# Performance work log

Hardware: AMD Instinct MI355X
Metric: run time of the kernel (lower is better)

Reference implementation:

```python
import jax, jax.numpy as jnp
import numpy as np

N = 50000      # nodes
E = 400000     # edges
IN = 128       # in_channels
HID = 64       # hidden_channels (per head)
H = 4          # heads
OUT = 10       # classes
G = 64         # graphs in batch


def setup_inputs() -> dict:
    key = jax.random.key(0)
    ks = jax.random.split(key, 32)
    s = 0.05
    inp = {
        "x": jax.random.normal(ks[0], (N, IN), dtype=jnp.float32),
        "edge_index": jax.random.randint(ks[1], (2, E), 0, N, dtype=jnp.int32),
        "batch": jnp.sort(jax.random.randint(ks[2], (N,), 0, G, dtype=jnp.int32)),
    }
    # TransformerConv layer 1 params (in=IN -> heads*HID)
    d1 = H * HID
    inp["Wq1"] = jax.random.normal(ks[3], (IN, d1)) * s
    inp["bq1"] = jnp.zeros((d1,), jnp.float32)
    inp["Wk1"] = jax.random.normal(ks[4], (IN, d1)) * s
    inp["bk1"] = jnp.zeros((d1,), jnp.float32)
    inp["Wv1"] = jax.random.normal(ks[5], (IN, d1)) * s
    inp["bv1"] = jnp.zeros((d1,), jnp.float32)
    inp["Ws1"] = jax.random.normal(ks[6], (IN, d1)) * s   # root/skip weight
    inp["bs1"] = jnp.zeros((d1,), jnp.float32)
    # TransformerConv layer 2 params (in=H*HID -> heads*HID)
    inp["Wq2"] = jax.random.normal(ks[7], (d1, d1)) * s
    inp["bq2"] = jnp.zeros((d1,), jnp.float32)
    inp["Wk2"] = jax.random.normal(ks[8], (d1, d1)) * s
    inp["bk2"] = jnp.zeros((d1,), jnp.float32)
    inp["Wv2"] = jax.random.normal(ks[9], (d1, d1)) * s
    inp["bv2"] = jnp.zeros((d1,), jnp.float32)
    inp["Ws2"] = jax.random.normal(ks[10], (d1, d1)) * s
    inp["bs2"] = jnp.zeros((d1,), jnp.float32)
    # final classifier
    inp["Wl"] = jax.random.normal(ks[11], (d1, OUT)) * s
    inp["bl"] = jnp.zeros((OUT,), jnp.float32)
    return inp


def transformer_conv(x, src, dst, Wq, bq, Wk, bk, Wv, bv, Ws, bs):
    """PyG TransformerConv (concat=True, root_weight=True, beta=None, eval mode).
    src = edge_index[0] (source j), dst = edge_index[1] (target i).
    """
    n = x.shape[0]
    q = (x @ Wq + bq).reshape(n, H, HID)
    k = (x @ Wk + bk).reshape(n, H, HID)
    v = (x @ Wv + bv).reshape(n, H, HID)
    # per-edge attention logits [E, H]
    alpha = jnp.einsum('ehc,ehc->eh', q[dst], k[src]) / np.sqrt(HID).astype(np.float32)
    # scatter-softmax over incoming edges of each target node
    amax = jax.ops.segment_max(alpha, dst, num_segments=n)           # [N, H], -inf for isolated
    ex = jnp.exp(alpha - amax[dst])                                   # [E, H]
    denom = jax.ops.segment_sum(ex, dst, num_segments=n) + 1e-16      # [N, H]
    w = ex / denom[dst]                                               # normalized alpha [E, H]
    # scatter-sum aggregation of weighted values
    out = jax.ops.segment_sum(w[:, :, None] * v[src], dst, num_segments=n)  # [N, H, HID]
    out = out.reshape(n, H * HID)
    return out + (x @ Ws + bs)  # root/skip connection


def reference(x, edge_index, batch,
              Wq1, bq1, Wk1, bk1, Wv1, bv1, Ws1, bs1,
              Wq2, bq2, Wk2, bk2, Wv2, bv2, Ws2, bs2,
              Wl, bl):
    src, dst = edge_index[0], edge_index[1]
    h = jax.nn.elu(transformer_conv(x, src, dst, Wq1, bq1, Wk1, bk1, Wv1, bv1, Ws1, bs1))
    h = jax.nn.elu(transformer_conv(h, src, dst, Wq2, bq2, Wk2, bk2, Wv2, bv2, Ws2, bs2))
    # global mean pool per graph
    sums = jax.ops.segment_sum(h, batch, num_segments=G)              # [G, H*HID]
    cnt = jax.ops.segment_sum(jnp.ones((h.shape[0],), h.dtype), batch, num_segments=G)
    pooled = sums / jnp.maximum(cnt, 1.0)[:, None]
    logits = pooled @ Wl + bl
    return jax.nn.log_softmax(logits, axis=-1)
```

## Files before the change

kernel.cpp:

```cpp
#include <hip/hip_runtime.h>
#include <math.h>

constexpr int NN   = 50000;
constexpr int NE   = 400000;
constexpr int INC  = 128;
constexpr int NH   = 4;
constexpr int D1   = 256;
constexpr int D4   = 1024;
constexpr int NOUT = 10;
constexpr int NG   = 64;
constexpr int NB_SCAN = (NN + 255) / 256;


typedef __attribute__((ext_vector_type(8))) short bf16x8;
typedef __attribute__((ext_vector_type(4))) float f32x4;
typedef __attribute__((ext_vector_type(2))) float f32x2;

__device__ __forceinline__ short f2b(float f) {
  union { float f; unsigned int i; } v; v.f = f;
  unsigned int x = v.i;
  return (short)((x + 0x7FFFu + ((x >> 16) & 1u)) >> 16);
}
__device__ __forceinline__ float b2f(short u) {
  union { unsigned int i; float f; } v; v.i = ((unsigned int)(unsigned short)u) << 16;
  return v.f;
}
__device__ __forceinline__ float4 ld4b(const short* p) {
  short4 u = *(const short4*)p;
  return make_float4(b2f(u.x), b2f(u.y), b2f(u.z), b2f(u.w));
}
__device__ __forceinline__ int cvt_pk_bf16(float lo, float hi) {
  int r;
  asm volatile("v_cvt_pk_bf16_f32 %0, %1, %2" : "=v"(r) : "v"(lo), "v"(hi));
  return r;
}
__device__ __forceinline__ int pk_fp8x4(float a, float b, float c, float d) {
  int v = __builtin_amdgcn_cvt_pk_fp8_f32(a, b, 0, false);
  v = __builtin_amdgcn_cvt_pk_fp8_f32(c, d, v, true);
  return v;
}

__device__ __forceinline__ void gld_lds16(const short* g, short* l) {
  __builtin_amdgcn_global_load_lds(
      (const __attribute__((address_space(1))) unsigned int*)g,
      (__attribute__((address_space(3))) unsigned int*)l, 16, 0, 0);
}

constexpr int CVT_XB  = (NN * INC / 4 + 255) / 256;
constexpr int CVT_W1B = (4 * D1 * INC / 8 + 255) / 256;
constexpr int CVT_W2B = (4 * D1 * D1 / 8 + 255) / 256;
constexpr int CVT_BB  = 8;
constexpr int CVT_DB  = (NN + 255) / 256;
constexpr int CVT_FB  = 1;
constexpr int CVT_SB  = (NG * D1 + 255) / 256;

__device__ __forceinline__ void wt_one8(const float* Wq, const float* Wk,
    const float* Wv, const float* Ws, short* Wt, int kbits, int i) {
  const int K = 1 << kbits;
  const int row = i >> (kbits - 3);
  const int k0 = (i & ((K >> 3) - 1)) << 3;
  int seg, n;
  if (row < 256)      { seg = 0; n = row; }
  else if (row < 768) { int j = row - 256, off = j & 7;
                        seg = (off >= 4) ? 2 : 1; n = (j >> 3) * 4 + (off & 3); }
  else                { seg = 3; n = row - 768; }
  const float* W = (seg == 0) ? Wq : (seg == 1) ? Wk : (seg == 2) ? Wv : Ws;
  short o[8];
#pragma unroll
  for (int kk = 0; kk < 8; kk++) o[kk] = f2b(W[(size_t)(k0 + kk) * D1 + n]);
  int4 pk;
  short* ps = (short*)&pk;
#pragma unroll
  for (int kk = 0; kk < 8; kk++) ps[kk] = o[kk];
  *(int4*)(Wt + (size_t)row * K + k0) = pk;
}

__global__ void cvt_all_k(const float* __restrict__ x, short* __restrict__ Xb,
    const float* __restrict__ Wq1, const float* __restrict__ Wk1,
    const float* __restrict__ Wv1, const float* __restrict__ Ws1,
    const float* __restrict__ Wq2, const float* __restrict__ Wk2,
    const float* __restrict__ Wv2, const float* __restrict__ Ws2,
    short* __restrict__ Wtc1, short* __restrict__ Wtc2,
    const float* __restrict__ bq1, const float* __restrict__ bk1,
    const float* __restrict__ bv1, const float* __restrict__ bs1,
    const float* __restrict__ bq2, const float* __restrict__ bk2,
    const float* __restrict__ bv2, const float* __restrict__ bs2,
    float* __restrict__ bc1, float* __restrict__ bc2,
    int* __restrict__ deg, unsigned int* __restrict__ desc,
    float* __restrict__ sums) {
  const int b = blockIdx.x;
  const int t = threadIdx.x;
  if (b < CVT_XB) {
    int i = (b * 256 + t) * 4;
    if (i >= NN * INC) return;
    float4 v = *(const float4*)(x + i);
    short4 o; o.x = f2b(v.x); o.y = f2b(v.y); o.z = f2b(v.z); o.w = f2b(v.w);
    *(short4*)(Xb + i) = o;
  } else if (b < CVT_XB + CVT_W1B) {
    int i = (b - CVT_XB) * 256 + t;
    if (i < 4 * D1 * INC / 8) wt_one8(Wq1, Wk1, Wv1, Ws1, Wtc1, 7, i);
  } else if (b < CVT_XB + CVT_W1B + CVT_W2B) {
    int i = (b - CVT_XB - CVT_W1B) * 256 + t;
    if (i < 4 * D1 * D1 / 8) wt_one8(Wq2, Wk2, Wv2, Ws2, Wtc2, 8, i);
  } else if (b < CVT_XB + CVT_W1B + CVT_W2B + CVT_BB) {
    int i = (b - CVT_XB - CVT_W1B - CVT_W2B) * 256 + t;
    if (i >= 2 * D4) return;
    int row = i & (D4 - 1);
    const float* bq = (i < D4) ? bq1 : bq2;
    const float* bk = (i < D4) ? bk1 : bk2;
    const float* bv = (i < D4) ? bv1 : bv2;
    const float* bs = (i < D4) ? bs1 : bs2;
    float v;
    if (row < 256) v = bq[row];
    else if (row < 768) {
      int j = row - 256, grp = j >> 3, off = j & 7;
      int ch = grp * 4 + (off & 3);
      v = (off < 4) ? bk[ch] : bv[ch];
    } else v = bs[row - 768];
    ((i < D4) ? bc1 : bc2)[row] = v;
  } else if (b < CVT_XB + CVT_W1B + CVT_W2B + CVT_BB + CVT_DB) {
    int i = (b - CVT_XB - CVT_W1B - CVT_W2B - CVT_BB) * 256 + t;
    if (i < NN) deg[i] = 0;
  } else if (b < CVT_XB + CVT_W1B + CVT_W2B + CVT_BB + CVT_DB + CVT_FB) {
    if (t < NB_SCAN) desc[t] = 0u;
  } else {
    int i = (b - CVT_XB - CVT_W1B - CVT_W2B - CVT_BB - CVT_DB - CVT_FB) * 256 + t;
    if (i < NG * D1) sums[i] = 0.f;
  }
}

__global__ void deg_count(const int* __restrict__ dst, int* __restrict__ deg) {
  int e = blockIdx.x * 256 + threadIdx.x;
  if (e < NE) atomicAdd(&deg[dst[e]], 1);
}

__global__ __launch_bounds__(256) void scan_k(const int* __restrict__ deg,
    const int* __restrict__ batch, unsigned int* __restrict__ desc,
    int* __restrict__ rowstart, int* __restrict__ cursor, int* __restrict__ gb) {
  const int b = blockIdx.x;
  const int t = threadIdx.x;
  if (b == NB_SCAN) {
    if (t > NG) return;
    int lo = 0, hi = NN;
    while (lo < hi) {
      int mid = (lo + hi) >> 1;
      if (batch[mid] < t) lo = mid + 1; else hi = mid;
    }
    gb[t] = lo;
    return;
  }
  __shared__ int sh[256];
  __shared__ int base_s;
  const int i = b * 256 + t;
  const int v = (i < NN) ? deg[i] : 0;
  sh[t] = v;
  __syncthreads();
  for (int off = 1; off < 256; off <<= 1) {
    int o = (t >= off) ? sh[t - off] : 0;
    __syncthreads();
    sh[t] += o;
    __syncthreads();
  }
  const int incl = sh[t];
  const int aggr = sh[255];
  if (t == 0)
    __hip_atomic_store(&desc[b], ((unsigned int)aggr << 2) | (b == 0 ? 2u : 1u),
                       __ATOMIC_RELEASE, __HIP_MEMORY_SCOPE_AGENT);
  if (b == 0) {
    if (t == 0) base_s = 0;
  } else if (t < 64) {
    int base = 0;
    int j = b - 1;
    for (;;) {
      const int idx = j - t;
      const unsigned int d = (idx >= 0)
          ? __hip_atomic_load(&desc[idx], __ATOMIC_ACQUIRE,
                              __HIP_MEMORY_SCOPE_AGENT)
          : 2u;
      const unsigned int st = d & 3u;
      const unsigned long long m_incl = __ballot(st == 2u);
      const unsigned long long m_inv  = __ballot(st == 0u);
      const int fi = m_incl ? (__ffsll((unsigned long long)m_incl) - 1) : 64;
      const int fv = m_inv  ? (__ffsll((unsigned long long)m_inv ) - 1) : 64;
      if (fi < fv) {
        int contrib = (t <= fi) ? (int)(d >> 2) : 0;
#pragma unroll
        for (int off = 1; off < 64; off <<= 1) contrib += __shfl_xor(contrib, off, 64);
        base += contrib;
        break;
      } else if (fv == 64) {
        int contrib = (int)(d >> 2);
#pragma unroll
        for (int off = 1; off < 64; off <<= 1) contrib += __shfl_xor(contrib, off, 64);
        base += contrib;
        j -= 64;
      } else {
        __builtin_amdgcn_s_sleep(1);
      }
    }
    if (t == 0) {
      __hip_atomic_store(&desc[b], ((unsigned int)(base + aggr) << 2) | 2u,
                         __ATOMIC_RELEASE, __HIP_MEMORY_SCOPE_AGENT);
      base_s = base;
    }
  }
  __syncthreads();
  const int excl = base_s + incl - v;
  if (i <= NN) rowstart[i] = excl;
  if (i < NN)  cursor[i]   = excl;
}

__global__ void scatter_k(const int* __restrict__ src, const int* __restrict__ dst,
    int* __restrict__ cursor, int* __restrict__ esrc) {
  int e = blockIdx.x * 256 + threadIdx.x;
  if (e >= NE) return;
  int d = dst[e];
  int pos = atomicAdd(&cursor[d], 1);
  esrc[pos] = src[e];
}

constexpr int CLDS = 136;

__global__ __launch_bounds__(256, 4) void gemm_mfma(
    const short* __restrict__ Xb, const short* __restrict__ Wt,
    const float* __restrict__ bias, short* __restrict__ QS,
    unsigned char* __restrict__ KV8, int M, int K) {
  __shared__ short smem[16384];
  const int bx = blockIdx.x;
  const int by = blockIdx.y;
  const int m_tile = (bx & 7) + (by << 3);
  const int n_tile = bx >> 3;
  const int m0 = m_tile * 128;
  if (m0 >= M) return;
  const int n0 = n_tile * 128;

  const int t    = threadIdx.x;
  const int lane = t & 63;
  const int wv   = t >> 6;
  const int wm   = (wv >> 1) * 64;
  const int wn   = (wv & 1) * 64;
  const int quad = lane >> 4;
  const int l16  = lane & 15;
  const int lrow = lane >> 2;
  const int lseg = lane & 3;

  const int swz_w = (lseg ^ ((lrow >> 1) & 3)) * 8;
  const int swz_r = (quad ^ ((l16 >> 1) & 3)) * 8;

  f32x4 acc[4][4] = {};

  {
#pragma unroll
    for (int j = 0; j < 2; ++j) {
      const int rb = (wv * 2 + j) * 16;
      int gm = m0 + rb + lrow;
      gm = gm < M ? gm : M - 1;
      gld_lds16(Xb + (size_t)gm * K + swz_w,              &smem[rb * 32]);
      gld_lds16(Wt + (size_t)(n0 + rb + lrow) * K + swz_w, &smem[4096 + rb * 32]);
    }
  }
  __syncthreads();

  int cur = 0;
  for (int k0 = 0; k0 < K; k0 += 32) {
    if (k0 + 32 < K) {
      short* An = &smem[(cur ^ 1) * 8192];
      short* Bn = &smem[(cur ^ 1) * 8192 + 4096];
#pragma unroll
      for (int j = 0; j < 2; ++j) {
        const int rb = (wv * 2 + j) * 16;
        int gm = m0 + rb + lrow;
        gm = gm < M ? gm : M - 1;
        gld_lds16(Xb + (size_t)gm * K + k0 + 32 + swz_w,              &An[rb * 32]);
        gld_lds16(Wt + (size_t)(n0 + rb + lrow) * K + k0 + 32 + swz_w, &Bn[rb * 32]);
      }
    }
    {
      const short* Ac = &smem[cur * 8192];
      const short* Bc = &smem[cur * 8192 + 4096];
      bf16x8 a[4], b[4];
#pragma unroll
      for (int mi = 0; mi < 4; mi++)
        a[mi] = *(const bf16x8*)(&Ac[(wm + mi * 16 + l16) * 32 + swz_r]);
#pragma unroll
      for (int nj = 0; nj < 4; nj++)
        b[nj] = *(const bf16x8*)(&Bc[(wn + nj * 16 + l16) * 32 + swz_r]);
#pragma unroll
      for (int mi = 0; mi < 4; mi++)
#pragma unroll
        for (int nj = 0; nj < 4; nj++)
          acc[mi][nj] = __builtin_amdgcn_mfma_f32_16x16x32_bf16(b[nj], a[mi], acc[mi][nj], 0, 0, 0);
    }
    __syncthreads();
    cur ^= 1;
  }

  const bool isKV = (n_tile >= 2) && (n_tile <= 5);
  float4 bz[4];
#pragma unroll
  for (int nj = 0; nj < 4; nj++)
    bz[nj] = *(const float4*)(bias + n0 + wn + nj * 16 + quad * 4);
  const int kv_base = n0 - 256;
  const int qs_base = (n_tile < 2) ? n0 : (n0 - 512);

#pragma unroll
  for (int p = 0; p < 2; ++p) {
    if ((wv >> 1) == p) {
      if (isKV) {
        unsigned char* cs = (unsigned char*)smem;
#pragma unroll
        for (int mi = 0; mi < 4; mi++) {
          const int row = mi * 16 + l16;
#pragma unroll
          for (int nj = 0; nj < 4; nj++) {
            const int colb = wn + nj * 16 + quad * 4;
            const int pk = pk_fp8x4(acc[mi][nj][0] + bz[nj].x, acc[mi][nj][1] + bz[nj].y,
                                    acc[mi][nj][2] + bz[nj].z, acc[mi][nj][3] + bz[nj].w);
            *(int*)(cs + row * 136 + colb) = pk;
          }
        }
      } else {
#pragma unroll
        for (int mi = 0; mi < 4; mi++) {
          const int row = mi * 16 + l16;
#pragma unroll
          for (int nj = 0; nj < 4; nj++) {
            const int col = wn + nj * 16 + quad * 4;
            int2 o;
            o.x = cvt_pk_bf16(acc[mi][nj][0] + bz[nj].x, acc[mi][nj][1] + bz[nj].y);
            o.y = cvt_pk_bf16(acc[mi][nj][2] + bz[nj].z, acc[mi][nj][3] + bz[nj].w);
            *(int2*)(&smem[row * CLDS + col]) = o;
          }
        }
      }
    }
    __syncthreads();
    if (isKV) {
      const unsigned char* cs = (const unsigned char*)smem;
#pragma unroll
      for (int it = 0; it < 4; ++it) {
        const int chunk = it * 256 + t;
        const int row = chunk >> 4;
        const int cb  = (chunk & 15) * 8;
        const int gm  = m0 + p * 64 + row;
        if (gm < M)
          *(int2*)(KV8 + (size_t)gm * 512 + kv_base + cb) = *(const int2*)(cs + row * 136 + cb);
      }
    } else {
#pragma unroll
      for (int it = 0; it < 4; ++it) {
        const int chunk = it * 256 + t;
        const int row = chunk >> 4;
        const int cc  = (chunk & 15) * 8;
        const int gm  = m0 + p * 64 + row;
        if (gm < M)
          *(int4*)(QS + (size_t)gm * 512 + qs_base + cc) = *(const int4*)(&smem[row * CLDS + cc]);
      }
    }
    if (p == 0) __syncthreads();
  }
}

__device__ __forceinline__ f32x2 cvt_lo(int x) { return __builtin_amdgcn_cvt_pk_f32_fp8(x, false); }
__device__ __forceinline__ f32x2 cvt_hi(int x) { return __builtin_amdgcn_cvt_pk_f32_fp8(x, true); }

template <int CTRL>
__device__ __forceinline__ float ror_add(float x) {
  int y = __builtin_amdgcn_update_dpp(0, __float_as_int(x), CTRL, 0xF, 0xF, true);
  return x + __int_as_float(y);
}
__device__ __forceinline__ float red16(float x) {
  x = ror_add<0x121>(x);
  x = ror_add<0x122>(x);
  x = ror_add<0x124>(x);
  x = ror_add<0x128>(x);
  return x;
}

#define SC2 (0.125f * 1.44269504088896341f)

__device__ __forceinline__ float edge_score(const int2 x, f32x2 q01, f32x2 q23,
                                            f32x2& vv01, f32x2& vv23) {
  f32x2 kk01 = cvt_lo(x.x), kk23 = cvt_hi(x.x);
  vv01 = cvt_lo(x.y); vv23 = cvt_hi(x.y);
  f32x2 dd = q01 * kk01;
  dd += q23 * kk23;
  return red16(dd.x + dd.y);
}

template <typename TOUT>
__device__ __forceinline__ void st1(TOUT* p, float v);
template <> __device__ __forceinline__ void st1<float>(float* p, float v) { *p = v; }
template <> __device__ __forceinline__ void st1<short>(short* p, float v) { *p = f2b(v); }

template <typename TOUT>
__global__ __launch_bounds__(256) void node_attn(
    const int* __restrict__ rowstart, const int* __restrict__ esrc,
    const short* __restrict__ QS, const unsigned char* __restrict__ KV8,
    TOUT* __restrict__ out) {
  const int nid = blockIdx.x * 4 + (threadIdx.x >> 6);
  if (nid >= NN) return;
  const int t  = threadIdx.x & 63;
  const int c0 = t * 4;
  const int r0 = __builtin_amdgcn_readfirstlane(rowstart[nid]);
  const int r1 = __builtin_amdgcn_readfirstlane(rowstart[nid + 1]);
  const short4 qu = *(const short4*)(QS + (size_t)nid * 512 + c0);
  const f32x2 q01 = {b2f(qu.x) * SC2, b2f(qu.y) * SC2};
  const f32x2 q23 = {b2f(qu.z) * SC2, b2f(qu.w) * SC2};
  const unsigned char* kvb = KV8 + t * 8;
  float m = -INFINITY, denom = 0.f;
  f32x2 a01 = {0.f, 0.f}, a23 = {0.f, 0.f};
  int r = r0;
  for (; r + 7 < r1; r += 8) {
    const int e0 = __builtin_amdgcn_readfirstlane(esrc[r + 0]);
    const int e1 = __builtin_amdgcn_readfirstlane(esrc[r + 1]);
    const int e2 = __builtin_amdgcn_readfirstlane(esrc[r + 2]);
    const int e3 = __builtin_amdgcn_readfirstlane(esrc[r + 3]);
    const int e4 = __builtin_amdgcn_readfirstlane(esrc[r + 4]);
    const int e5 = __builtin_amdgcn_readfirstlane(esrc[r + 5]);
    const int e6 = __builtin_amdgcn_readfirstlane(esrc[r + 6]);
    const int e7 = __builtin_amdgcn_readfirstlane(esrc[r + 7]);
    const int2 x0 = *(const int2*)(kvb + (size_t)e0 * 512);
    const int2 x1 = *(const int2*)(kvb + (size_t)e1 * 512);
    const int2 x2 = *(const int2*)(kvb + (size_t)e2 * 512);
    const int2 x3 = *(const int2*)(kvb + (size_t)e3 * 512);
    const int2 x4 = *(const int2*)(kvb + (size_t)e4 * 512);
    const int2 x5 = *(const int2*)(kvb + (size_t)e5 * 512);
    const int2 x6 = *(const int2*)(kvb + (size_t)e6 * 512);
    const int2 x7 = *(const int2*)(kvb + (size_t)e7 * 512);
    f32x2 v01_0, v23_0, v01_1, v23_1, v01_2, v23_2, v01_3, v23_3;
    f32x2 v01_4, v23_4, v01_5, v23_5, v01_6, v23_6, v01_7, v23_7;
    const float s0 = edge_score(x0, q01, q23, v01_0, v23_0);
    const float s1 = edge_score(x1, q01, q23, v01_1, v23_1);
    const float s2 = edge_score(x2, q01, q23, v01_2, v23_2);
    const float s3 = edge_score(x3, q01, q23, v01_3, v23_3);
    const float s4 = edge_score(x4, q01, q23, v01_4, v23_4);
    const float s5 = edge_score(x5, q01, q23, v01_5, v23_5);
    const float s6 = edge_score(x6, q01, q23, v01_6, v23_6);
    const float s7 = edge_score(x7, q01, q23, v01_7, v23_7);
    const float t01 = fmaxf(s0, s1), t23 = fmaxf(s2, s3);
    const float t45 = fmaxf(s4, s5), t67 = fmaxf(s6, s7);
    const float nm = fmaxf(fmaxf(m, fmaxf(t01, t23)), fmaxf(t45, t67));
    const float sc  = exp2f(m - nm);
    const float ex0 = exp2f(s0 - nm);
    const float ex1 = exp2f(s1 - nm);
    const float ex2 = exp2f(s2 - nm);
    const float ex3 = exp2f(s3 - nm);
    const float ex4 = exp2f(s4 - nm);
    const float ex5 = exp2f(s5 - nm);
    const float ex6 = exp2f(s6 - nm);
    const float ex7 = exp2f(s7 - nm);
    denom = denom * sc + ((ex0 + ex1) + (ex2 + ex3)) + ((ex4 + ex5) + (ex6 + ex7));
    const f32x2 scv = {sc, sc};
    a01 = a01 * scv; a23 = a23 * scv;
    a01 += f32x2{ex0, ex0} * v01_0; a23 += f32x2{ex0, ex0} * v23_0;
    a01 += f32x2{ex1, ex1} * v01_1; a23 += f32x2{ex1, ex1} * v23_1;
    a01 += f32x2{ex2, ex2} * v01_2; a23 += f32x2{ex2, ex2} * v23_2;
    a01 += f32x2{ex3, ex3} * v01_3; a23 += f32x2{ex3, ex3} * v23_3;
    a01 += f32x2{ex4, ex4} * v01_4; a23 += f32x2{ex4, ex4} * v23_4;
    a01 += f32x2{ex5, ex5} * v01_5; a23 += f32x2{ex5, ex5} * v23_5;
    a01 += f32x2{ex6, ex6} * v01_6; a23 += f32x2{ex6, ex6} * v23_6;
    a01 += f32x2{ex7, ex7} * v01_7; a23 += f32x2{ex7, ex7} * v23_7;
    m = nm;
  }
  for (; r + 3 < r1; r += 4) {
    const int e0 = __builtin_amdgcn_readfirstlane(esrc[r + 0]);
    const int e1 = __builtin_amdgcn_readfirstlane(esrc[r + 1]);
    const int e2 = __builtin_amdgcn_readfirstlane(esrc[r + 2]);
    const int e3 = __builtin_amdgcn_readfirstlane(esrc[r + 3]);
    const int2 x0 = *(const int2*)(kvb + (size_t)e0 * 512);
    const int2 x1 = *(const int2*)(kvb + (size_t)e1 * 512);
    const int2 x2 = *(const int2*)(kvb + (size_t)e2 * 512);
    const int2 x3 = *(const int2*)(kvb + (size_t)e3 * 512);
    f32x2 v01_0, v23_0, v01_1, v23_1, v01_2, v23_2, v01_3, v23_3;
    const float s0 = edge_score(x0, q01, q23, v01_0, v23_0);
    const float s1 = edge_score(x1, q01, q23, v01_1, v23_1);
    const float s2 = edge_score(x2, q01, q23, v01_2, v23_2);
    const float s3 = edge_score(x3, q01, q23, v01_3, v23_3);
    const float nm = fmaxf(fmaxf(m, fmaxf(s0, s1)), fmaxf(s2, s3));
    const float sc  = exp2f(m - nm);
    const float ex0 = exp2f(s0 - nm);
    const float ex1 = exp2f(s1 - nm);
    const float ex2 = exp2f(s2 - nm);
    const float ex3 = exp2f(s3 - nm);
    denom = denom * sc + ex0 + ex1 + ex2 + ex3;
    const f32x2 scv = {sc, sc};
    a01 = a01 * scv; a23 = a23 * scv;
    a01 += f32x2{ex0, ex0} * v01_0; a23 += f32x2{ex0, ex0} * v23_0;
    a01 += f32x2{ex1, ex1} * v01_1; a23 += f32x2{ex1, ex1} * v23_1;
    a01 += f32x2{ex2, ex2} * v01_2; a23 += f32x2{ex2, ex2} * v23_2;
    a01 += f32x2{ex3, ex3} * v01_3; a23 += f32x2{ex3, ex3} * v23_3;
    m = nm;
  }
  for (; r < r1; r++) {
    const int e0 = __builtin_amdgcn_readfirstlane(esrc[r]);
    const int2 x0 = *(const int2*)(kvb + (size_t)e0 * 512);
    f32x2 v01_0, v23_0;
    const float s0 = edge_score(x0, q01, q23, v01_0, v23_0);
    const float nm = fmaxf(m, s0);
    const float sc  = exp2f(m - nm);
    const float ex0 = exp2f(s0 - nm);
    denom = denom * sc + ex0;
    const f32x2 scv = {sc, sc};
    a01 = a01 * scv; a23 = a23 * scv;
    a01 += f32x2{ex0, ex0} * v01_0; a23 += f32x2{ex0, ex0} * v23_0;
    m = nm;
  }
  const float inv = 1.0f / (denom + 1e-16f);
  const float4 sk = ld4b(QS + (size_t)nid * 512 + 256 + c0);
  float o0 = a01.x * inv + sk.x;
  float o1 = a01.y * inv + sk.y;
  float o2 = a23.x * inv + sk.z;
  float o3 = a23.y * inv + sk.w;
  o0 = o0 > 0.f ? o0 : expm1f(o0);
  o1 = o1 > 0.f ? o1 : expm1f(o1);
  o2 = o2 > 0.f ? o2 : expm1f(o2);
  o3 = o3 > 0.f ? o3 : expm1f(o3);
  TOUT* p = out + (size_t)nid * D1 + c0;
  st1<TOUT>(p + 0, o0); st1<TOUT>(p + 1, o1);
  st1<TOUT>(p + 2, o2); st1<TOUT>(p + 3, o3);
}

__global__ __launch_bounds__(256) void pool_k(const short* __restrict__ h,
    const int* __restrict__ batch, const int* __restrict__ gb,
    float* __restrict__ sums) {
  const int c = threadIdx.x;
  const int n0 = blockIdx.x * 64;
  const int n1 = min(n0 + 64, NN);
  const int g0 = batch[n0];
  const int g1 = batch[n1 - 1];
  for (int g = g0; g <= g1; ++g) {
    const int a = max(gb[g], n0);
    const int b = min(gb[g + 1], n1);
    if (b <= a) continue;
    float s0 = 0.f, s1 = 0.f, s2 = 0.f, s3 = 0.f;
    int n = a;
    for (; n + 3 < b; n += 4) {
      s0 += b2f(h[(size_t)(n + 0) * D1 + c]);
      s1 += b2f(h[(size_t)(n + 1) * D1 + c]);
      s2 += b2f(h[(size_t)(n + 2) * D1 + c]);
      s3 += b2f(h[(size_t)(n + 3) * D1 + c]);
    }
    for (; n < b; ++n) s0 += b2f(h[(size_t)n * D1 + c]);
    atomicAdd(&sums[(size_t)g * D1 + c], (s0 + s1) + (s2 + s3));
  }
}

__global__ __launch_bounds__(640) void head_k(const float* __restrict__ sums,
    const int* __restrict__ gb, const float* __restrict__ Wl,
    const float* __restrict__ bl, float* __restrict__ out) {
  __shared__ float logits[NG][NOUT];
  const int t = threadIdx.x;
  if (t < NG * NOUT) {
    int g = t / NOUT, o = t % NOUT;
    float inv = 1.0f / fmaxf((float)(gb[g + 1] - gb[g]), 1.0f);
    float acc = 0.f;
    for (int k = 0; k < D1; k++) acc += sums[(size_t)g * D1 + k] * Wl[k * NOUT + o];
    logits[g][o] = acc * inv + bl[o];
  }
  __syncthreads();
  if (t < NG) {
    float mx = -INFINITY;
#pragma unroll
    for (int o = 0; o < NOUT; o++) mx = fmaxf(mx, logits[t][o]);
    float s = 0.f;
#pragma unroll
    for (int o = 0; o < NOUT; o++) s += __expf(logits[t][o] - mx);
    float lse = mx + logf(s);
#pragma unroll
    for (int o = 0; o < NOUT; o++) out[t * NOUT + o] = logits[t][o] - lse;
  }
}

extern "C" void kernel_launch(void* const* d_in, const int* in_sizes, int n_in,
                              void* d_out, int out_size, void* d_ws, size_t ws_size,
                              hipStream_t stream) {
  const float* x   = (const float*)d_in[0];
  const int* ei    = (const int*)d_in[1];
  const int* batch = (const int*)d_in[2];
  const float* Wq1 = (const float*)d_in[3];  const float* bq1 = (const float*)d_in[4];
  const float* Wk1 = (const float*)d_in[5];  const float* bk1 = (const float*)d_in[6];
  const float* Wv1 = (const float*)d_in[7];  const float* bv1 = (const float*)d_in[8];
  const float* Ws1 = (const float*)d_in[9];  const float* bs1 = (const float*)d_in[10];
  const float* Wq2 = (const float*)d_in[11]; const float* bq2 = (const float*)d_in[12];
  const float* Wk2 = (const float*)d_in[13]; const float* bk2 = (const float*)d_in[14];
  const float* Wv2 = (const float*)d_in[15]; const float* bv2 = (const float*)d_in[16];
  const float* Ws2 = (const float*)d_in[17]; const float* bs2 = (const float*)d_in[18];
  const float* Wl  = (const float*)d_in[19]; const float* bl  = (const float*)d_in[20];

  const int* srcIdx = ei;
  const int* dstIdx = ei + NE;

  float* ws = (float*)d_ws;
  const size_t SZ_NODE = (size_t)NN * D1;
  short* H2b  = (short*)ws;
  float* sums = ws + SZ_NODE;
  float* bc1  = sums + (size_t)NG * D1;
  float* bc2  = bc1 + D4;
  short* Xb   = (short*)(bc2 + D4);
  short* H1b  = Xb + (size_t)NN * INC;
  short* QS   = H1b + SZ_NODE;
  short* Wtc1 = QS + (size_t)NN * 512;
  short* Wtc2 = Wtc1 + (size_t)D4 * INC;
  unsigned char* KV8 = (unsigned char*)(Wtc2 + (size_t)D4 * D1);
  int* ip      = (int*)(KV8 + (size_t)NN * 512);
  int* deg     = ip;
  unsigned int* desc = (unsigned int*)(deg + NN);
  int* rowstart= (int*)(desc + 256);
  int* cursor  = rowstart + NN + 1;
  int* esrc    = cursor + NN;
  int* gb      = esrc + NE;

  const int mtiles = (NN + 127) / 128;
  const dim3 gemmGrid(64, (mtiles + 7) / 8);
  const int edgeBlocks = (NE + 255) / 256;
  const int aggBlocks  = (NN + 3) / 4;
  const int cvtBlocks  = CVT_XB + CVT_W1B + CVT_W2B + CVT_BB + CVT_DB + CVT_FB + CVT_SB;

  cvt_all_k<<<cvtBlocks, 256, 0, stream>>>(x, Xb,
      Wq1, Wk1, Wv1, Ws1, Wq2, Wk2, Wv2, Ws2, Wtc1, Wtc2,
      bq1, bk1, bv1, bs1, bq2, bk2, bv2, bs2, bc1, bc2, deg, desc, sums);

  deg_count<<<edgeBlocks, 256, 0, stream>>>(dstIdx, deg);
  scan_k<<<NB_SCAN + 1, 256, 0, stream>>>(deg, batch, desc, rowstart, cursor, gb);
  scatter_k<<<edgeBlocks, 256, 0, stream>>>(srcIdx, dstIdx, cursor, esrc);

  gemm_mfma<<<gemmGrid, 256, 0, stream>>>(Xb, Wtc1, bc1, QS, KV8, NN, INC);
  node_attn<short><<<aggBlocks, 256, 0, stream>>>(rowstart, esrc, QS, KV8, H1b);

  gemm_mfma<<<gemmGrid, 256, 0, stream>>>(H1b, Wtc2, bc2, QS, KV8, NN, D1);
  node_attn<short><<<aggBlocks, 256, 0, stream>>>(rowstart, esrc, QS, KV8, H2b);

  pool_k<<<(NN + 63) / 64, 256, 0, stream>>>(H2b, batch, gb, sums);
  head_k<<<1, 640, 0, stream>>>(sums, gb, Wl, bl, (float*)d_out);
}
```

Baseline: 336.2 us.

## Drop softmax max tracking, vectorize edge kernels, coalesce weight transpose

```diff
diff --git a/kernel.cpp b/kernel.cpp
--- a/kernel.cpp
+++ b/kernel.cpp
@@ -47,33 +47,11 @@
 }
 
 constexpr int CVT_XB  = (NN * INC / 4 + 255) / 256;
-constexpr int CVT_W1B = (4 * D1 * INC / 8 + 255) / 256;
-constexpr int CVT_W2B = (4 * D1 * D1 / 8 + 255) / 256;
+constexpr int CVT_WTB = 48;
 constexpr int CVT_BB  = 8;
 constexpr int CVT_DB  = (NN + 255) / 256;
 constexpr int CVT_FB  = 1;
 constexpr int CVT_SB  = (NG * D1 + 255) / 256;
-
-__device__ __forceinline__ void wt_one8(const float* Wq, const float* Wk,
-    const float* Wv, const float* Ws, short* Wt, int kbits, int i) {
-  const int K = 1 << kbits;
-  const int row = i >> (kbits - 3);
-  const int k0 = (i & ((K >> 3) - 1)) << 3;
-  int seg, n;
-  if (row < 256)      { seg = 0; n = row; }
-  else if (row < 768) { int j = row - 256, off = j & 7;
-                        seg = (off >= 4) ? 2 : 1; n = (j >> 3) * 4 + (off & 3); }
-  else                { seg = 3; n = row - 768; }
-  const float* W = (seg == 0) ? Wq : (seg == 1) ? Wk : (seg == 2) ? Wv : Ws;
-  short o[8];
-#pragma unroll
-  for (int kk = 0; kk < 8; kk++) o[kk] = f2b(W[(size_t)(k0 + kk) * D1 + n]);
-  int4 pk;
-  short* ps = (short*)&pk;
-#pragma unroll
-  for (int kk = 0; kk < 8; kk++) ps[kk] = o[kk];
-  *(int4*)(Wt + (size_t)row * K + k0) = pk;
-}
 
 __global__ void cvt_all_k(const float* __restrict__ x, short* __restrict__ Xb,
     const float* __restrict__ Wq1, const float* __restrict__ Wk1,
@@ -96,14 +74,30 @@
     float4 v = *(const float4*)(x + i);
     short4 o; o.x = f2b(v.x); o.y = f2b(v.y); o.z = f2b(v.z); o.w = f2b(v.w);
     *(short4*)(Xb + i) = o;
-  } else if (b < CVT_XB + CVT_W1B) {
-    int i = (b - CVT_XB) * 256 + t;
-    if (i < 4 * D1 * INC / 8) wt_one8(Wq1, Wk1, Wv1, Ws1, Wtc1, 7, i);
-  } else if (b < CVT_XB + CVT_W1B + CVT_W2B) {
-    int i = (b - CVT_XB - CVT_W1B) * 256 + t;
-    if (i < 4 * D1 * D1 / 8) wt_one8(Wq2, Wk2, Wv2, Ws2, Wtc2, 8, i);
-  } else if (b < CVT_XB + CVT_W1B + CVT_W2B + CVT_BB) {
-    int i = (b - CVT_XB - CVT_W1B - CVT_W2B) * 256 + t;
+  } else if (b < CVT_XB + CVT_WTB) {
+    const int w = b - CVT_XB;
+    const bool l1 = (w < 16);
+    const int mat   = l1 ? (w >> 2) : ((w - 16) >> 3);
+    const int panel = l1 ? (w & 3)  : ((w - 16) & 7);
+    const int K = l1 ? INC : D1;
+    const int k0 = panel * 32;
+    const float* Wm[8] = {Wq1, Wk1, Wv1, Ws1, Wq2, Wk2, Wv2, Ws2};
+    const float* W = Wm[(l1 ? 0 : 4) + mat];
+    short* Wt = l1 ? Wtc1 : Wtc2;
+    int row;
+    if (mat == 0)      row = t;
+    else if (mat == 3) row = 768 + t;
+    else               row = 256 + (t >> 2) * 8 + ((mat == 2) ? 4 : 0) + (t & 3);
+    int4 pk[4];
+    short* ps = (short*)pk;
+#pragma unroll
+    for (int kk = 0; kk < 32; ++kk)
+      ps[kk] = f2b(W[(size_t)(k0 + kk) * D1 + t]);
+#pragma unroll
+    for (int j = 0; j < 4; ++j)
+      *(int4*)(Wt + (size_t)row * K + k0 + j * 8) = pk[j];
+  } else if (b < CVT_XB + CVT_WTB + CVT_BB) {
+    int i = (b - CVT_XB - CVT_WTB) * 256 + t;
     if (i >= 2 * D4) return;
     int row = i & (D4 - 1);
     const float* bq = (i < D4) ? bq1 : bq2;
@@ -118,20 +112,28 @@
       v = (off < 4) ? bk[ch] : bv[ch];
     } else v = bs[row - 768];
     ((i < D4) ? bc1 : bc2)[row] = v;
-  } else if (b < CVT_XB + CVT_W1B + CVT_W2B + CVT_BB + CVT_DB) {
-    int i = (b - CVT_XB - CVT_W1B - CVT_W2B - CVT_BB) * 256 + t;
+  } else if (b < CVT_XB + CVT_WTB + CVT_BB + CVT_DB) {
+    int i = (b - CVT_XB - CVT_WTB - CVT_BB) * 256 + t;
     if (i < NN) deg[i] = 0;
-  } else if (b < CVT_XB + CVT_W1B + CVT_W2B + CVT_BB + CVT_DB + CVT_FB) {
+  } else if (b < CVT_XB + CVT_WTB + CVT_BB + CVT_DB + CVT_FB) {
     if (t < NB_SCAN) desc[t] = 0u;
   } else {
-    int i = (b - CVT_XB - CVT_W1B - CVT_W2B - CVT_BB - CVT_DB - CVT_FB) * 256 + t;
+    int i = (b - CVT_XB - CVT_WTB - CVT_BB - CVT_DB - CVT_FB) * 256 + t;
     if (i < NG * D1) sums[i] = 0.f;
   }
 }
 
 __global__ void deg_count(const int* __restrict__ dst, int* __restrict__ deg) {
-  int e = blockIdx.x * 256 + threadIdx.x;
-  if (e < NE) atomicAdd(&deg[dst[e]], 1);
+  int e = (blockIdx.x * 256 + threadIdx.x) * 4;
+  if (e + 3 < NE) {
+    const int4 d = *(const int4*)(dst + e);
+    atomicAdd(&deg[d.x], 1);
+    atomicAdd(&deg[d.y], 1);
+    atomicAdd(&deg[d.z], 1);
+    atomicAdd(&deg[d.w], 1);
+  } else {
+    for (; e < NE; ++e) atomicAdd(&deg[dst[e]], 1);
+  }
 }
 
 __global__ __launch_bounds__(256) void scan_k(const int* __restrict__ deg,
@@ -212,11 +214,17 @@
 
 __global__ void scatter_k(const int* __restrict__ src, const int* __restrict__ dst,
     int* __restrict__ cursor, int* __restrict__ esrc) {
-  int e = blockIdx.x * 256 + threadIdx.x;
-  if (e >= NE) return;
-  int d = dst[e];
-  int pos = atomicAdd(&cursor[d], 1);
-  esrc[pos] = src[e];
+  int e = (blockIdx.x * 256 + threadIdx.x) * 4;
+  if (e + 3 < NE) {
+    const int4 s4 = *(const int4*)(src + e);
+    const int4 d4 = *(const int4*)(dst + e);
+    esrc[atomicAdd(&cursor[d4.x], 1)] = s4.x;
+    esrc[atomicAdd(&cursor[d4.y], 1)] = s4.y;
+    esrc[atomicAdd(&cursor[d4.z], 1)] = s4.z;
+    esrc[atomicAdd(&cursor[d4.w], 1)] = s4.w;
+  } else {
+    for (; e < NE; ++e) esrc[atomicAdd(&cursor[dst[e]], 1)] = src[e];
+  }
 }
 
 constexpr int CLDS = 136;
@@ -408,7 +416,7 @@
   const f32x2 q01 = {b2f(qu.x) * SC2, b2f(qu.y) * SC2};
   const f32x2 q23 = {b2f(qu.z) * SC2, b2f(qu.w) * SC2};
   const unsigned char* kvb = KV8 + t * 8;
-  float m = -INFINITY, denom = 0.f;
+  float denom = 0.f;
   f32x2 a01 = {0.f, 0.f}, a23 = {0.f, 0.f};
   int r = r0;
   for (; r + 7 < r1; r += 8) {
@@ -430,29 +438,15 @@
     const int2 x7 = *(const int2*)(kvb + (size_t)e7 * 512);
     f32x2 v01_0, v23_0, v01_1, v23_1, v01_2, v23_2, v01_3, v23_3;
     f32x2 v01_4, v23_4, v01_5, v23_5, v01_6, v23_6, v01_7, v23_7;
-    const float s0 = edge_score(x0, q01, q23, v01_0, v23_0);
-    const float s1 = edge_score(x1, q01, q23, v01_1, v23_1);
-    const float s2 = edge_score(x2, q01, q23, v01_2, v23_2);
-    const float s3 = edge_score(x3, q01, q23, v01_3, v23_3);
-    const float s4 = edge_score(x4, q01, q23, v01_4, v23_4);
-    const float s5 = edge_score(x5, q01, q23, v01_5, v23_5);
-    const float s6 = edge_score(x6, q01, q23, v01_6, v23_6);
-    const float s7 = edge_score(x7, q01, q23, v01_7, v23_7);
-    const float t01 = fmaxf(s0, s1), t23 = fmaxf(s2, s3);
-    const float t45 = fmaxf(s4, s5), t67 = fmaxf(s6, s7);
-    const float nm = fmaxf(fmaxf(m, fmaxf(t01, t23)), fmaxf(t45, t67));
-    const float sc  = exp2f(m - nm);
-    const float ex0 = exp2f(s0 - nm);
-    const float ex1 = exp2f(s1 - nm);
-    const float ex2 = exp2f(s2 - nm);
-    const float ex3 = exp2f(s3 - nm);
-    const float ex4 = exp2f(s4 - nm);
-    const float ex5 = exp2f(s5 - nm);
-    const float ex6 = exp2f(s6 - nm);
-    const float ex7 = exp2f(s7 - nm);
-    denom = denom * sc + ((ex0 + ex1) + (ex2 + ex3)) + ((ex4 + ex5) + (ex6 + ex7));
-    const f32x2 scv = {sc, sc};
-    a01 = a01 * scv; a23 = a23 * scv;
+    const float ex0 = exp2f(edge_score(x0, q01, q23, v01_0, v23_0));
+    const float ex1 = exp2f(edge_score(x1, q01, q23, v01_1, v23_1));
+    const float ex2 = exp2f(edge_score(x2, q01, q23, v01_2, v23_2));
+    const float ex3 = exp2f(edge_score(x3, q01, q23, v01_3, v23_3));
+    const float ex4 = exp2f(edge_score(x4, q01, q23, v01_4, v23_4));
+    const float ex5 = exp2f(edge_score(x5, q01, q23, v01_5, v23_5));
+    const float ex6 = exp2f(edge_score(x6, q01, q23, v01_6, v23_6));
+    const float ex7 = exp2f(edge_score(x7, q01, q23, v01_7, v23_7));
+    denom += ((ex0 + ex1) + (ex2 + ex3)) + ((ex4 + ex5) + (ex6 + ex7));
     a01 += f32x2{ex0, ex0} * v01_0; a23 += f32x2{ex0, ex0} * v23_0;
     a01 += f32x2{ex1, ex1} * v01_1; a23 += f32x2{ex1, ex1} * v23_1;
     a01 += f32x2{ex2, ex2} * v01_2; a23 += f32x2{ex2, ex2} * v23_2;
@@ -461,7 +455,6 @@
     a01 += f32x2{ex5, ex5} * v01_5; a23 += f32x2{ex5, ex5} * v23_5;
     a01 += f32x2{ex6, ex6} * v01_6; a23 += f32x2{ex6, ex6} * v23_6;
     a01 += f32x2{ex7, ex7} * v01_7; a23 += f32x2{ex7, ex7} * v23_7;
-    m = nm;
   }
   for (; r + 3 < r1; r += 4) {
     const int e0 = __builtin_amdgcn_readfirstlane(esrc[r + 0]);
@@ -473,38 +466,23 @@
     const int2 x2 = *(const int2*)(kvb + (size_t)e2 * 512);
     const int2 x3 = *(const int2*)(kvb + (size_t)e3 * 512);
     f32x2 v01_0, v23_0, v01_1, v23_1, v01_2, v23_2, v01_3, v23_3;
-    const float s0 = edge_score(x0, q01, q23, v01_0, v23_0);
-    const float s1 = edge_score(x1, q01, q23, v01_1, v23_1);
-    const float s2 = edge_score(x2, q01, q23, v01_2, v23_2);
-    const float s3 = edge_score(x3, q01, q23, v01_3, v23_3);
-    const float nm = fmaxf(fmaxf(m, fmaxf(s0, s1)), fmaxf(s2, s3));
-    const float sc  = exp2f(m - nm);
-    const float ex0 = exp2f(s0 - nm);
-    const float ex1 = exp2f(s1 - nm);
-    const float ex2 = exp2f(s2 - nm);
-    const float ex3 = exp2f(s3 - nm);
-    denom = denom * sc + ex0 + ex1 + ex2 + ex3;
-    const f32x2 scv = {sc, sc};
-    a01 = a01 * scv; a23 = a23 * scv;
+    const float ex0 = exp2f(edge_score(x0, q01, q23, v01_0, v23_0));
+    const float ex1 = exp2f(edge_score(x1, q01, q23, v01_1, v23_1));
+    const float ex2 = exp2f(edge_score(x2, q01, q23, v01_2, v23_2));
+    const float ex3 = exp2f(edge_score(x3, q01, q23, v01_3, v23_3));
+    denom += (ex0 + ex1) + (ex2 + ex3);
     a01 += f32x2{ex0, ex0} * v01_0; a23 += f32x2{ex0, ex0} * v23_0;
     a01 += f32x2{ex1, ex1} * v01_1; a23 += f32x2{ex1, ex1} * v23_1;
     a01 += f32x2{ex2, ex2} * v01_2; a23 += f32x2{ex2, ex2} * v23_2;
     a01 += f32x2{ex3, ex3} * v01_3; a23 += f32x2{ex3, ex3} * v23_3;
-    m = nm;
   }
   for (; r < r1; r++) {
     const int e0 = __builtin_amdgcn_readfirstlane(esrc[r]);
     const int2 x0 = *(const int2*)(kvb + (size_t)e0 * 512);
     f32x2 v01_0, v23_0;
-    const float s0 = edge_score(x0, q01, q23, v01_0, v23_0);
-    const float nm = fmaxf(m, s0);
-    const float sc  = exp2f(m - nm);
-    const float ex0 = exp2f(s0 - nm);
-    denom = denom * sc + ex0;
-    const f32x2 scv = {sc, sc};
-    a01 = a01 * scv; a23 = a23 * scv;
+    const float ex0 = exp2f(edge_score(x0, q01, q23, v01_0, v23_0));
+    denom += ex0;
     a01 += f32x2{ex0, ex0} * v01_0; a23 += f32x2{ex0, ex0} * v23_0;
-    m = nm;
   }
   const float inv = 1.0f / (denom + 1e-16f);
   const float4 sk = ld4b(QS + (size_t)nid * 512 + 256 + c0);
@@ -613,17 +591,17 @@
 
   const int mtiles = (NN + 127) / 128;
   const dim3 gemmGrid(64, (mtiles + 7) / 8);
-  const int edgeBlocks = (NE + 255) / 256;
+  const int edgeBlocks4 = (NE / 4 + 255) / 256;
   const int aggBlocks  = (NN + 3) / 4;
-  const int cvtBlocks  = CVT_XB + CVT_W1B + CVT_W2B + CVT_BB + CVT_DB + CVT_FB + CVT_SB;
+  const int cvtBlocks  = CVT_XB + CVT_WTB + CVT_BB + CVT_DB + CVT_FB + CVT_SB;
 
   cvt_all_k<<<cvtBlocks, 256, 0, stream>>>(x, Xb,
       Wq1, Wk1, Wv1, Ws1, Wq2, Wk2, Wv2, Ws2, Wtc1, Wtc2,
       bq1, bk1, bv1, bs1, bq2, bk2, bv2, bs2, bc1, bc2, deg, desc, sums);
 
-  deg_count<<<edgeBlocks, 256, 0, stream>>>(dstIdx, deg);
+  deg_count<<<edgeBlocks4, 256, 0, stream>>>(dstIdx, deg);
   scan_k<<<NB_SCAN + 1, 256, 0, stream>>>(deg, batch, desc, rowstart, cursor, gb);
-  scatter_k<<<edgeBlocks, 256, 0, stream>>>(srcIdx, dstIdx, cursor, esrc);
+  scatter_k<<<edgeBlocks4, 256, 0, stream>>>(srcIdx, dstIdx, cursor, esrc);
 
   gemm_mfma<<<gemmGrid, 256, 0, stream>>>(Xb, Wtc1, bc1, QS, KV8, NN, INC);
   node_attn<short><<<aggBlocks, 256, 0, stream>>>(rowstart, esrc, QS, KV8, H1b);
```

Result: no change. 332.4 us (-1.1%).
